# Kernel optimization log

Measured on AMD Instinct MI355X. Metric: run time of the kernel, lower is better.

The kernel has to match this reference:

```python
import jax, jax.numpy as jnp
import numpy as np

DIM = 512
HEADS = 8
DHEAD = 64
INNER = HEADS * DHEAD
CHUNK = 8
GAMMA = 1.0
EPS = 1e-8
LN_EPS = 1e-5


def setup_inputs() -> dict:
    key = jax.random.key(0)
    ks = jax.random.split(key, 10)
    B, N = 64, 256
    return {
        "q": jax.random.normal(ks[0], (B, N, DIM), jnp.float32),
        "k": jax.random.normal(ks[1], (B, N, DIM), jnp.float32),
        "v": jax.random.normal(ks[2], (B, N, DIM), jnp.float32),
        "ln_gamma": jnp.ones((DIM,), jnp.float32),
        "ln_beta": jnp.zeros((DIM,), jnp.float32),
        "W_in": jax.random.normal(ks[3], (DIM, INNER), jnp.float32) / np.sqrt(DIM),
        "W_out": jax.random.normal(ks[4], (INNER, DIM), jnp.float32) / np.sqrt(INNER),
        "b_out": jnp.zeros((DIM,), jnp.float32),
        "cov_logit": jnp.asarray(0.6, jnp.float32),
        "var_logit": jnp.asarray(0.2, jnp.float32),
        "use_advanced": 1,
    }


def _layernorm(x, g, b):
    mu = jnp.mean(x, axis=-1, keepdims=True)
    var = jnp.mean(jnp.square(x - mu), axis=-1, keepdims=True)
    return (x - mu) * jax.lax.rsqrt(var + LN_EPS) * g + b


def _transform(t, ln_gamma, ln_beta, W_in):
    # [B,N,dim] -> [h,B,N,d]
    B, N, _ = t.shape
    f = _layernorm(t, ln_gamma, ln_beta) @ W_in
    return f.reshape(B, N, HEADS, DHEAD).transpose(2, 0, 1, 3)


def _chunk_stats(E):
    # E: [M, N, d], chunks of size CHUNK over M. Returns per-chunk scalars V, C of shape [M//CHUNK].
    M, N, d = E.shape
    nc = M // CHUNK
    Ec = E.reshape(nc, CHUNK, N, d)
    # variance component: torch.var is unbiased (ddof=1) over seq dim
    sigma = jnp.sqrt(jnp.var(Ec, axis=2, ddof=1) + EPS)  # [nc, CHUNK, d]
    V = jnp.mean(jax.nn.relu(GAMMA - sigma), axis=(1, 2))  # [nc]
    # covariance component: per-sample off-diagonal energy, averaged per chunk
    centered = Ec - jnp.mean(Ec, axis=2, keepdims=True)
    cov = jnp.einsum("csni,csnj->csij", centered, centered) / (N - 1)  # [nc,CHUNK,d,d]
    total = jnp.sum(jnp.square(cov), axis=(2, 3))
    diag = jnp.sum(jnp.square(jnp.diagonal(cov, axis1=2, axis2=3)), axis=2)
    C = jnp.mean((total - diag) / d, axis=1)  # [nc]
    return V, C


def reference(q, k, v, ln_gamma, ln_beta, W_in, W_out, b_out, cov_logit, var_logit, use_advanced):
    f_q = _transform(q, ln_gamma, ln_beta, W_in)  # [h,B,N,d]
    f_k = _transform(k, ln_gamma, ln_beta, W_in)
    f_v = _transform(v, ln_gamma, ln_beta, W_in)
    h, B, N, d = f_q.shape

    # cosine similarity
    dots_qk = jnp.einsum("hbnd,hbmd->hbnm", f_q, f_k)
    qn = jnp.linalg.norm(f_q, axis=-1)  # [h,B,N]
    kn = jnp.linalg.norm(f_k, axis=-1)
    cosine_sim = dots_qk / (qn[..., :, None] * kn[..., None, :])

    if use_advanced:
        Vq, Cq = _chunk_stats(f_q.reshape(h * B, N, d))
        Vk, Ck = _chunk_stats(f_k.reshape(h * B, N, d))
        var_component = jnp.repeat(Vq * Vk, CHUNK).reshape(h, B, 1, 1)
        cov_component = jnp.repeat(Cq * Ck, CHUNK).reshape(h, B, 1, 1)
    else:
        qc = f_q - jnp.mean(f_q, axis=-1, keepdims=True)
        kc = f_k - jnp.mean(f_k, axis=-1, keepdims=True)
        cov_component = jnp.einsum("hbnd,hbmd->hbnm", qc, kc) / d
        q_var = jnp.var(f_q, axis=-1, ddof=1, keepdims=True)  # [h,B,N,1]
        k_var = jnp.var(f_k, axis=-1, ddof=1, keepdims=True)
        var_component = (q_var * jnp.swapaxes(k_var, -1, -2)) / d

    cov_w = jax.nn.sigmoid(cov_logit)
    var_w = jax.nn.sigmoid(var_logit)
    cos_w = 1.0 - cov_w - var_w
    dots = cos_w * cosine_sim + cov_w * cov_component + var_w * var_component
    out = jnp.einsum("hbnm,hbmd->hbnd", dots, f_v)
    out = out.transpose(1, 2, 0, 3).reshape(B, N, h * d)
    return out @ W_out + b_out
```

## Files before the change

### kernel.cpp

```cpp
#include <hip/hip_runtime.h>
#include <cstdint>
#include <cstddef>

#define DIM    512
#define HEADS  8
#define DHEAD  64
#define NSEQ   256
#define BATCH  64
#define NROWS  (BATCH * NSEQ)
#define HB     (HEADS * BATCH)

typedef unsigned short u16;
typedef __bf16 bf16x8 __attribute__((ext_vector_type(8)));
typedef float  f32x4  __attribute__((ext_vector_type(4)));

__device__ __forceinline__ float sigmoidf_(float x) { return 1.0f / (1.0f + expf(-x)); }

__device__ __forceinline__ u16 f2bf(float f) {
    union { float f; unsigned u; } a; a.f = f;
    return (u16)((a.u + 0x7fffu + ((a.u >> 16) & 1u)) >> 16);
}

__device__ __forceinline__ void gload16(const void* g, void* l) {
    __builtin_amdgcn_global_load_lds((const __attribute__((address_space(1))) void*)g,
                                     (__attribute__((address_space(3))) void*)l, 16, 0, 0);
}

__global__ __launch_bounds__(256)
void ln_cast_kernel(const float* __restrict__ x, const float* __restrict__ gam,
                    const float* __restrict__ bet, u16* __restrict__ out)
{
    const int wid = threadIdx.x >> 6, lane = threadIdx.x & 63;
    const int row = blockIdx.x * 4 + wid;
    const float* xr = x + (size_t)row * DIM;
    float4 a = *(const float4*)(xr + lane * 8);
    float4 b = *(const float4*)(xr + lane * 8 + 4);
    float v[8] = {a.x, a.y, a.z, a.w, b.x, b.y, b.z, b.w};
    float s = 0.f;
#pragma unroll
    for (int i = 0; i < 8; ++i) s += v[i];
#pragma unroll
    for (int o = 32; o > 0; o >>= 1) s += __shfl_xor(s, o, 64);
    const float mu = s * (1.f / DIM);
    float sq = 0.f;
#pragma unroll
    for (int i = 0; i < 8; ++i) { float d = v[i] - mu; sq += d * d; }
#pragma unroll
    for (int o = 32; o > 0; o >>= 1) sq += __shfl_xor(sq, o, 64);
    const float rstd = rsqrtf(sq * (1.f / DIM) + 1e-5f);
    float4 g0 = *(const float4*)(gam + lane * 8), g1 = *(const float4*)(gam + lane * 8 + 4);
    float4 b0 = *(const float4*)(bet + lane * 8), b1 = *(const float4*)(bet + lane * 8 + 4);
    float gv[8] = {g0.x, g0.y, g0.z, g0.w, g1.x, g1.y, g1.z, g1.w};
    float bv[8] = {b0.x, b0.y, b0.z, b0.w, b1.x, b1.y, b1.z, b1.w};
    union { u16 h[8]; uint4 u; } o16;
#pragma unroll
    for (int i = 0; i < 8; ++i) o16.h[i] = f2bf((v[i] - mu) * rstd * gv[i] + bv[i]);
    *(uint4*)(out + (size_t)row * DIM + lane * 8) = o16.u;
}

__global__ __launch_bounds__(256)
void transpose_cast_kernel(const float* __restrict__ W, u16* __restrict__ WT)
{
    __shared__ float tile[64][65];
    const int t = threadIdx.x;
    const int bx = blockIdx.x * 64, by = blockIdx.y * 64;
#pragma unroll
    for (int i = 0; i < 16; ++i) {
        int idx = i * 256 + t, r = idx >> 6, c = idx & 63;
        tile[r][c] = W[(size_t)(by + r) * DIM + bx + c];
    }
    __syncthreads();
#pragma unroll
    for (int i = 0; i < 16; ++i) {
        int idx = i * 256 + t, r = idx >> 6, c = idx & 63;
        WT[(size_t)(bx + r) * DIM + by + c] = f2bf(tile[c][r]);
    }
}

template <int MODE>
__global__ __launch_bounds__(256)
void mfma_gemm_kernel(const u16* __restrict__ A, const u16* __restrict__ BT,
                      const float* __restrict__ bias, float* __restrict__ C,
                      u16* __restrict__ FT, u16* __restrict__ Fseq)
{
    __shared__ u16 As[128 * 32];
    __shared__ u16 Bs[128 * 32];
    const int t = threadIdx.x, lane = t & 63, w = t >> 6;
    const int wr = w >> 1, wc = w & 1;
    const int r0 = blockIdx.x * 128, c0 = blockIdx.y * 128;
    const int cl = lane & 15, q = lane >> 4;

    f32x4 acc[4][4];
#pragma unroll
    for (int i = 0; i < 4; ++i)
#pragma unroll
        for (int j = 0; j < 4; ++j) acc[i][j] = (f32x4){0.f, 0.f, 0.f, 0.f};

    for (int k0 = 0; k0 < DIM; k0 += 32) {
#pragma unroll
        for (int i = 0; i < 2; ++i) {
            int idx = i * 256 + t;
            int row = idx >> 2, ch = idx & 3;
            gload16(A  + (size_t)(r0 + row) * DIM + k0 + ch * 8, As + idx * 8);
            gload16(BT + (size_t)(c0 + row) * DIM + k0 + ch * 8, Bs + idx * 8);
        }
        __syncthreads();
        bf16x8 af[4], bfr[4];
#pragma unroll
        for (int mi = 0; mi < 4; ++mi)
            af[mi] = *(const bf16x8*)(As + (wr * 64 + mi * 16 + cl) * 32 + q * 8);
#pragma unroll
        for (int ni = 0; ni < 4; ++ni)
            bfr[ni] = *(const bf16x8*)(Bs + (wc * 64 + ni * 16 + cl) * 32 + q * 8);
#pragma unroll
        for (int mi = 0; mi < 4; ++mi)
#pragma unroll
            for (int ni = 0; ni < 4; ++ni)
                acc[mi][ni] = __builtin_amdgcn_mfma_f32_16x16x32_bf16(af[mi], bfr[ni],
                                                                      acc[mi][ni], 0, 0, 0);
        __syncthreads();
    }
#pragma unroll
    for (int mi = 0; mi < 4; ++mi) {
        int row0 = r0 + wr * 64 + mi * 16 + q * 4;
#pragma unroll
        for (int ni = 0; ni < 4; ++ni) {
            int col = c0 + wc * 64 + ni * 16 + cl;
            if (MODE == 1) {
                float bv = bias[col];
#pragma unroll
                for (int r = 0; r < 4; ++r)
                    C[(size_t)(row0 + r) * DIM + col] = acc[mi][ni][r] + bv;
            } else {
                union { u16 h[4]; ushort4 u; } h4;
#pragma unroll
                for (int r = 0; r < 4; ++r) h4.h[r] = f2bf(acc[mi][ni][r]);
                int tns = row0 >> 14, b = (row0 >> 8) & 63, n = row0 & 255;
                *(ushort4*)(FT + (((size_t)(tns * 64 + b) * 512 + col) * 256 + n)) = h4.u;
                if (row0 < NROWS) {
#pragma unroll
                    for (int r = 0; r < 4; ++r)
                        Fseq[(size_t)(row0 + r) * DIM + col] = h4.h[r];
                }
            }
        }
    }
}

__global__ __launch_bounds__(256)
void stats_kernel(const u16* __restrict__ FT, float* __restrict__ norms,
                  float2* __restrict__ vc)
{
    __shared__ u16 ET[64 * 264];
    __shared__ float mu[64];
    __shared__ float red[4][64];
    __shared__ float wr3[4][3];
    const int hb = blockIdx.x, tns = blockIdx.y, h = hb >> 6, b = hb & 63;
    const int t = threadIdx.x, lane = t & 63, w = t >> 6, cl = lane & 15, q = lane >> 4;
    const size_t Fb = ((size_t)(tns * 64 + b) * 512 + h * 64) * 256;

#pragma unroll
    for (int i = 0; i < 8; ++i) {
        int idx = t + 256 * i;
        int row = idx >> 5, ch = idx & 31;
        *(bf16x8*)(ET + row * 264 + ch * 8) =
            *(const bf16x8*)(FT + Fb + (size_t)row * 256 + ch * 8);
    }
    __syncthreads();

    {
        float s = 0.f;
#pragma unroll
        for (int d = 0; d < 64; ++d) {
            float x = (float)*(const __bf16*)(ET + d * 264 + t);
            s += x * x;
        }
        norms[((size_t)tns * HB + hb) * 256 + t] = sqrtf(s);
    }
    {
        int d = t & 63, part = t >> 6;
        float s = 0.f;
#pragma unroll
        for (int i = 0; i < 8; ++i) {
            bf16x8 v8 = *(const bf16x8*)(ET + d * 264 + part * 64 + i * 8);
#pragma unroll
            for (int j = 0; j < 8; ++j) s += (float)v8[j];
        }
        red[part][d] = s;
    }
    __syncthreads();
    if (t < 64) mu[t] = (red[0][t] + red[1][t] + red[2][t] + red[3][t]) * (1.f / 256.f);
    __syncthreads();

    f32x4 g[4];
#pragma unroll
    for (int nj = 0; nj < 4; ++nj) g[nj] = (f32x4){0.f, 0.f, 0.f, 0.f};
#pragma unroll
    for (int ks = 0; ks < 8; ++ks) {
        bf16x8 af = *(const bf16x8*)(ET + (16 * w + cl) * 264 + ks * 32 + q * 8);
#pragma unroll
        for (int nj = 0; nj < 4; ++nj) {
            bf16x8 bfr = *(const bf16x8*)(ET + (16 * nj + cl) * 264 + ks * 32 + q * 8);
            g[nj] = __builtin_amdgcn_mfma_f32_16x16x32_bf16(af, bfr, g[nj], 0, 0, 0);
        }
    }
    float t2 = 0.f, d2 = 0.f, vs = 0.f;
#pragma unroll
    for (int nj = 0; nj < 4; ++nj) {
        int j = 16 * nj + cl;
        float mj = mu[j];
#pragma unroll
        for (int r = 0; r < 4; ++r) {
            int i = 16 * w + 4 * q + r;
            float gc = (g[nj][r] - 256.f * mu[i] * mj) * (1.f / 255.f);
            float g2 = gc * gc;
            t2 += g2;
            if (i == j) {
                d2 += g2;
                float sig = sqrtf(gc + 1e-8f);
                vs += fmaxf(1.f - sig, 0.f);
            }
        }
    }
#pragma unroll
    for (int o = 32; o > 0; o >>= 1) {
        t2 += __shfl_xor(t2, o, 64);
        d2 += __shfl_xor(d2, o, 64);
        vs += __shfl_xor(vs, o, 64);
    }
    if (lane == 0) { wr3[w][0] = t2; wr3[w][1] = d2; wr3[w][2] = vs; }
    __syncthreads();
    if (t == 0) {
        float T = 0.f, D = 0.f, V = 0.f;
        for (int i = 0; i < 4; ++i) { T += wr3[i][0]; D += wr3[i][1]; V += wr3[i][2]; }
        vc[(size_t)tns * HB + hb] = make_float2(V * (1.f / 64.f), (T - D) * (1.f / 64.f));
    }
}

__global__ void combine_kernel(const float2* __restrict__ vc, const float* __restrict__ cov_logit,
                               const float* __restrict__ var_logit, float* __restrict__ s_out)
{
    int hb = threadIdx.x + blockIdx.x * blockDim.x;
    if (hb >= HB) return;
    int base = hb & ~7;
    float vq = 0, cq = 0, vk = 0, ck = 0;
#pragma unroll
    for (int m = 0; m < 8; ++m) {
        float2 a = vc[base + m];      vq += a.x; cq += a.y;
        float2 b = vc[HB + base + m]; vk += b.x; ck += b.y;
    }
    float cw = sigmoidf_(*cov_logit), vw = sigmoidf_(*var_logit);
    s_out[hb] = (cw * cq * ck + vw * vq * vk) * (1.f / 64.f);
}

__global__ __launch_bounds__(256)
void attn_kernel(const u16* __restrict__ FT, const u16* __restrict__ Fseq,
                 const float* __restrict__ norms, const float* __restrict__ s_arr,
                 const float* __restrict__ cov_logit, const float* __restrict__ var_logit,
                 u16* __restrict__ G)
{
    __shared__ u16 pool[256 * 72];
    __shared__ u16 MT[64 * 72];
    __shared__ float invq[256], invk[256], sv[64];
    const int hb = blockIdx.x, h = hb >> 6, b = hb & 63;
    const int t = threadIdx.x, lane = t & 63, w = t >> 6, cl = lane & 15, q = lane >> 4;
    u16* KT = pool;
    u16* VT = pool + 64 * 136;

    invq[t] = 1.f / norms[((size_t)0 * HB + hb) * 256 + t];
    invk[t] = 1.f / norms[((size_t)1 * HB + hb) * 256 + t];
    __syncthreads();

    const size_t FTk = ((size_t)(1 * 64 + b) * 512 + h * 64) * 256;
    const size_t FTv = ((size_t)(2 * 64 + b) * 512 + h * 64) * 256;
    f32x4 acc1[4];
#pragma unroll
    for (int nj = 0; nj < 4; ++nj) acc1[nj] = (f32x4){0.f, 0.f, 0.f, 0.f};
    float sp[4] = {0.f, 0.f, 0.f, 0.f};

    for (int c = 0; c < 2; ++c) {
#pragma unroll
        for (int i = 0; i < 4; ++i) {
            int idx = t + 256 * i;
            int row = idx >> 4, ch = idx & 15;
            int n0 = c * 128 + ch * 8;
            bf16x8 kv = *(const bf16x8*)(FT + FTk + (size_t)row * 256 + n0);
            bf16x8 vv = *(const bf16x8*)(FT + FTv + (size_t)row * 256 + n0);
            bf16x8 ksc;
#pragma unroll
            for (int j = 0; j < 8; ++j) ksc[j] = (__bf16)((float)kv[j] * invk[n0 + j]);
            *(bf16x8*)(KT + row * 136 + ch * 8) = ksc;
            *(bf16x8*)(VT + row * 136 + ch * 8) = vv;
        }
        __syncthreads();
#pragma unroll
        for (int ks = 0; ks < 4; ++ks) {
            bf16x8 af = *(const bf16x8*)(KT + (16 * w + cl) * 136 + ks * 32 + q * 8);
#pragma unroll
            for (int nj = 0; nj < 4; ++nj) {
                bf16x8 bfr = *(const bf16x8*)(VT + (16 * nj + cl) * 136 + ks * 32 + q * 8);
                if (w == 0) {
                    float s = 0.f;
#pragma unroll
                    for (int j = 0; j < 8; ++j) s += (float)bfr[j];
                    sp[nj] += s;
                }
                acc1[nj] = __builtin_amdgcn_mfma_f32_16x16x32_bf16(af, bfr, acc1[nj], 0, 0, 0);
            }
        }
        __syncthreads();
    }
    if (w == 0) {
#pragma unroll
        for (int nj = 0; nj < 4; ++nj) {
            float s = sp[nj];
            s += __shfl_xor(s, 16, 64);
            s += __shfl_xor(s, 32, 64);
            if (q == 0) sv[16 * nj + cl] = s;
        }
    }
#pragma unroll
    for (int nj = 0; nj < 4; ++nj)
#pragma unroll
        for (int r = 0; r < 4; ++r)
            MT[(16 * nj + cl) * 72 + 16 * w + 4 * q + r] = f2bf(acc1[nj][r]);
    __syncthreads();

    const float cw = sigmoidf_(*cov_logit), vw = sigmoidf_(*var_logit);
    const float cosw = 1.f - cw - vw;
    const float s_hb = s_arr[hb];
    f32x4 acc2[4][4];
#pragma unroll
    for (int mi = 0; mi < 4; ++mi)
#pragma unroll
        for (int nj = 0; nj < 4; ++nj) acc2[mi][nj] = (f32x4){0.f, 0.f, 0.f, 0.f};
    const size_t Fq = (size_t)(b * 256) * DIM + h * 64;
#pragma unroll
    for (int ks2 = 0; ks2 < 2; ++ks2) {
        bf16x8 bfm[4];
#pragma unroll
        for (int nj = 0; nj < 4; ++nj)
            bfm[nj] = *(const bf16x8*)(MT + (16 * nj + cl) * 72 + ks2 * 32 + q * 8);
#pragma unroll
        for (int mi = 0; mi < 4; ++mi) {
            bf16x8 aq = *(const bf16x8*)(Fseq + Fq +
                         (size_t)(64 * w + 16 * mi + cl) * DIM + ks2 * 32 + q * 8);
#pragma unroll
            for (int nj = 0; nj < 4; ++nj)
                acc2[mi][nj] = __builtin_amdgcn_mfma_f32_16x16x32_bf16(aq, bfm[nj],
                                                                       acc2[mi][nj], 0, 0, 0);
        }
    }
    __syncthreads();
    u16* Os = pool;
#pragma unroll
    for (int mi = 0; mi < 4; ++mi) {
        int nbase = 64 * w + 16 * mi + 4 * q;
#pragma unroll
        for (int nj = 0; nj < 4; ++nj) {
            int j = 16 * nj + cl;
            float svj = sv[j];
#pragma unroll
            for (int r = 0; r < 4; ++r) {
                float o = cosw * acc2[mi][nj][r] * invq[nbase + r] + s_hb * svj;
                Os[(nbase + r) * 72 + j] = f2bf(o);
            }
        }
    }
    __syncthreads();
#pragma unroll
    for (int i = 0; i < 8; ++i) {
        int cidx = t + 256 * i;
        int row = cidx >> 3, ch = cidx & 7;
        *(uint4*)(G + (size_t)(b * 256 + row) * DIM + h * 64 + ch * 8) =
            *(const uint4*)(Os + row * 72 + ch * 8);
    }
}

extern "C" void kernel_launch(void* const* d_in, const int* in_sizes, int n_in,
                              void* d_out, int out_size, void* d_ws, size_t ws_size,
                              hipStream_t stream)
{
    const float* q         = (const float*)d_in[0];
    const float* k         = (const float*)d_in[1];
    const float* v         = (const float*)d_in[2];
    const float* ln_g      = (const float*)d_in[3];
    const float* ln_b      = (const float*)d_in[4];
    const float* W_in      = (const float*)d_in[5];
    const float* W_out     = (const float*)d_in[6];
    const float* b_out     = (const float*)d_in[7];
    const float* cov_logit = (const float*)d_in[8];
    const float* var_logit = (const float*)d_in[9];
    float* out = (float*)d_out;

    char* base = (char*)d_ws;
    u16*    Abf   = (u16*)base;
    u16*    WT    = (u16*)(base + 50331648);
    u16*    FT    = (u16*)(base + 51380224);
    u16*    Fseq  = (u16*)(base + 101711872);
    float*  norms = (float*)(base + 118489088);
    float2* vc    = (float2*)(base + 119537664);
    float*  s_arr = (float*)(base + 119545856);
    u16*    Gb    = Abf;

    transpose_cast_kernel<<<dim3(8, 8), 256, 0, stream>>>(W_in, WT);
    transpose_cast_kernel<<<dim3(8, 8), 256, 0, stream>>>(W_out, WT + 512 * 512);

    const float* in3[3] = {q, k, v};
    for (int tns = 0; tns < 3; ++tns)
        ln_cast_kernel<<<dim3(NROWS / 4), 256, 0, stream>>>(in3[tns], ln_g, ln_b,
                                                            Abf + (size_t)tns * NROWS * DIM);
    mfma_gemm_kernel<0><<<dim3(3 * NROWS / 128, 4), 256, 0, stream>>>(
        Abf, WT, nullptr, nullptr, FT, Fseq);

    stats_kernel<<<dim3(HB, 2), 256, 0, stream>>>(FT, norms, vc);
    combine_kernel<<<dim3(1), 512, 0, stream>>>(vc, cov_logit, var_logit, s_arr);
    attn_kernel<<<dim3(HB), 256, 0, stream>>>(FT, Fseq, norms, s_arr,
                                              cov_logit, var_logit, Gb);
    mfma_gemm_kernel<1><<<dim3(NROWS / 128, 4), 256, 0, stream>>>(
        Gb, WT + 512 * 512, b_out, out, nullptr, nullptr);
}
```

Baseline: 256.1 us.

## Fuse layernorm into input projection GEMM and stage epilogue stores through LDS

Removes the separate layernorm-to-bf16 kernel. The input GEMM now computes per-row mean and rstd in a prologue and normalizes fp32 activations as it loads A tiles into LDS. The GEMM epilogue stages results through a padded LDS tile so the transposed FT and sequence-major Fseq writes become coalesced 16-byte stores. The combine kernel is folded into attention and the two weight transposes are merged into one launch. The aim is to cut the bf16 activation round-trip and launch overhead, at the cost of reading each input row once per column block (4x) without async loads, plus a one-pass variance formula.

```diff
diff --git a/kernel.cpp b/kernel.cpp
--- a/kernel.cpp
+++ b/kernel.cpp
@@ -27,43 +27,14 @@
 }
 
 __global__ __launch_bounds__(256)
-void ln_cast_kernel(const float* __restrict__ x, const float* __restrict__ gam,
-                    const float* __restrict__ bet, u16* __restrict__ out)
-{
-    const int wid = threadIdx.x >> 6, lane = threadIdx.x & 63;
-    const int row = blockIdx.x * 4 + wid;
-    const float* xr = x + (size_t)row * DIM;
-    float4 a = *(const float4*)(xr + lane * 8);
-    float4 b = *(const float4*)(xr + lane * 8 + 4);
-    float v[8] = {a.x, a.y, a.z, a.w, b.x, b.y, b.z, b.w};
-    float s = 0.f;
-#pragma unroll
-    for (int i = 0; i < 8; ++i) s += v[i];
-#pragma unroll
-    for (int o = 32; o > 0; o >>= 1) s += __shfl_xor(s, o, 64);
-    const float mu = s * (1.f / DIM);
-    float sq = 0.f;
-#pragma unroll
-    for (int i = 0; i < 8; ++i) { float d = v[i] - mu; sq += d * d; }
-#pragma unroll
-    for (int o = 32; o > 0; o >>= 1) sq += __shfl_xor(sq, o, 64);
-    const float rstd = rsqrtf(sq * (1.f / DIM) + 1e-5f);
-    float4 g0 = *(const float4*)(gam + lane * 8), g1 = *(const float4*)(gam + lane * 8 + 4);
-    float4 b0 = *(const float4*)(bet + lane * 8), b1 = *(const float4*)(bet + lane * 8 + 4);
-    float gv[8] = {g0.x, g0.y, g0.z, g0.w, g1.x, g1.y, g1.z, g1.w};
-    float bv[8] = {b0.x, b0.y, b0.z, b0.w, b1.x, b1.y, b1.z, b1.w};
-    union { u16 h[8]; uint4 u; } o16;
-#pragma unroll
-    for (int i = 0; i < 8; ++i) o16.h[i] = f2bf((v[i] - mu) * rstd * gv[i] + bv[i]);
-    *(uint4*)(out + (size_t)row * DIM + lane * 8) = o16.u;
-}
-
-__global__ __launch_bounds__(256)
-void transpose_cast_kernel(const float* __restrict__ W, u16* __restrict__ WT)
+void transpose_cast_kernel(const float* __restrict__ W0, const float* __restrict__ W1,
+                           u16* __restrict__ WT)
 {
     __shared__ float tile[64][65];
     const int t = threadIdx.x;
     const int bx = blockIdx.x * 64, by = blockIdx.y * 64;
+    const float* W = blockIdx.z ? W1 : W0;
+    u16* dst = WT + (size_t)blockIdx.z * 512 * 512;
 #pragma unroll
     for (int i = 0; i < 16; ++i) {
         int idx = i * 256 + t, r = idx >> 6, c = idx & 63;
@@ -73,22 +44,54 @@
 #pragma unroll
     for (int i = 0; i < 16; ++i) {
         int idx = i * 256 + t, r = idx >> 6, c = idx & 63;
-        WT[(size_t)(bx + r) * DIM + by + c] = f2bf(tile[c][r]);
-    }
-}
-
-template <int MODE>
+        dst[(size_t)(bx + r) * DIM + by + c] = f2bf(tile[c][r]);
+    }
+}
+
 __global__ __launch_bounds__(256)
-void mfma_gemm_kernel(const u16* __restrict__ A, const u16* __restrict__ BT,
-                      const float* __restrict__ bias, float* __restrict__ C,
-                      u16* __restrict__ FT, u16* __restrict__ Fseq)
+void fused_in_gemm_kernel(const float* __restrict__ qp, const float* __restrict__ kp,
+                          const float* __restrict__ vp, const float* __restrict__ gam,
+                          const float* __restrict__ bet, const u16* __restrict__ BT,
+                          u16* __restrict__ FT, u16* __restrict__ Fseq)
 {
     __shared__ u16 As[128 * 32];
     __shared__ u16 Bs[128 * 32];
+    __shared__ u16 Ct[128 * 136];
+    __shared__ float2 lnst[128];
     const int t = threadIdx.x, lane = t & 63, w = t >> 6;
     const int wr = w >> 1, wc = w & 1;
     const int r0 = blockIdx.x * 128, c0 = blockIdx.y * 128;
-    const int cl = lane & 15, q = lane >> 4;
+    const int tns = r0 >> 14;
+    const float* X = (tns == 0) ? qp : (tns == 1) ? kp : vp;
+    const int lr0 = r0 & 16383;
+    const int cl = lane & 15, qd = lane >> 4;
+
+    {
+        const int rl = t >> 4, l16 = t & 15;
+        for (int rg = 0; rg < 8; ++rg) {
+            int row = rg * 16 + rl;
+            const float* xr = X + (size_t)(lr0 + row) * DIM;
+            float s = 0.f, sq = 0.f;
+#pragma unroll
+            for (int j2 = 0; j2 < 8; ++j2) {
+                float4 xv = *(const float4*)(xr + l16 * 4 + j2 * 64);
+                s += xv.x + xv.y + xv.z + xv.w;
+                sq += xv.x * xv.x + xv.y * xv.y + xv.z * xv.z + xv.w * xv.w;
+            }
+#pragma unroll
+            for (int o = 8; o > 0; o >>= 1) { s += __shfl_xor(s, o, 64); sq += __shfl_xor(sq, o, 64); }
+            if (l16 == 0) {
+                float mu = s * (1.f / DIM);
+                float var = sq * (1.f / DIM) - mu * mu;
+                lnst[row] = make_float2(mu, rsqrtf(var + 1e-5f));
+            }
+        }
+    }
+    __syncthreads();
+    float2 ms[4];
+#pragma unroll
+    for (int i = 0; i < 4; ++i) ms[i] = lnst[(t >> 3) + 32 * i];
+    const int c4 = (t & 7) * 4;
 
     f32x4 acc[4][4];
 #pragma unroll
@@ -97,21 +100,33 @@
         for (int j = 0; j < 4; ++j) acc[i][j] = (f32x4){0.f, 0.f, 0.f, 0.f};
 
     for (int k0 = 0; k0 < DIM; k0 += 32) {
+        float4 g4 = *(const float4*)(gam + k0 + c4);
+        float4 b4 = *(const float4*)(bet + k0 + c4);
 #pragma unroll
         for (int i = 0; i < 2; ++i) {
-            int idx = i * 256 + t;
-            int row = idx >> 2, ch = idx & 3;
-            gload16(A  + (size_t)(r0 + row) * DIM + k0 + ch * 8, As + idx * 8);
+            int idx = i * 256 + t, row = idx >> 2, ch = idx & 3;
             gload16(BT + (size_t)(c0 + row) * DIM + k0 + ch * 8, Bs + idx * 8);
         }
+#pragma unroll
+        for (int i = 0; i < 4; ++i) {
+            int row = (t >> 3) + 32 * i;
+            float4 xv = *(const float4*)(X + (size_t)(lr0 + row) * DIM + k0 + c4);
+            float2 m = ms[i];
+            union { u16 h[4]; ushort4 u; } h4;
+            h4.h[0] = f2bf((xv.x - m.x) * m.y * g4.x + b4.x);
+            h4.h[1] = f2bf((xv.y - m.x) * m.y * g4.y + b4.y);
+            h4.h[2] = f2bf((xv.z - m.x) * m.y * g4.z + b4.z);
+            h4.h[3] = f2bf((xv.w - m.x) * m.y * g4.w + b4.w);
+            *(ushort4*)(As + row * 32 + c4) = h4.u;
+        }
         __syncthreads();
         bf16x8 af[4], bfr[4];
 #pragma unroll
         for (int mi = 0; mi < 4; ++mi)
-            af[mi] = *(const bf16x8*)(As + (wr * 64 + mi * 16 + cl) * 32 + q * 8);
+            af[mi] = *(const bf16x8*)(As + (wr * 64 + mi * 16 + cl) * 32 + qd * 8);
 #pragma unroll
         for (int ni = 0; ni < 4; ++ni)
-            bfr[ni] = *(const bf16x8*)(Bs + (wc * 64 + ni * 16 + cl) * 32 + q * 8);
+            bfr[ni] = *(const bf16x8*)(Bs + (wc * 64 + ni * 16 + cl) * 32 + qd * 8);
 #pragma unroll
         for (int mi = 0; mi < 4; ++mi)
 #pragma unroll
@@ -120,30 +135,46 @@
                                                                       acc[mi][ni], 0, 0, 0);
         __syncthreads();
     }
+
+    if (tns == 0) {
+#pragma unroll
+        for (int mi = 0; mi < 4; ++mi) {
+            int lrow = wr * 64 + mi * 16 + qd * 4;
+#pragma unroll
+            for (int ni = 0; ni < 4; ++ni) {
+                int lcol = wc * 64 + ni * 16 + cl;
+#pragma unroll
+                for (int r = 0; r < 4; ++r)
+                    Ct[(lrow + r) * 136 + lcol] = f2bf(acc[mi][ni][r]);
+            }
+        }
+        __syncthreads();
+#pragma unroll
+        for (int i = 0; i < 8; ++i) {
+            int idx = t + 256 * i, row = idx >> 4, ch = idx & 15;
+            *(uint4*)(Fseq + (size_t)(lr0 + row) * DIM + c0 + ch * 8) =
+                *(const uint4*)(Ct + row * 136 + ch * 8);
+        }
+        __syncthreads();
+    }
 #pragma unroll
     for (int mi = 0; mi < 4; ++mi) {
-        int row0 = r0 + wr * 64 + mi * 16 + q * 4;
+        int lrow = wr * 64 + mi * 16 + qd * 4;
 #pragma unroll
         for (int ni = 0; ni < 4; ++ni) {
-            int col = c0 + wc * 64 + ni * 16 + cl;
-            if (MODE == 1) {
-                float bv = bias[col];
-#pragma unroll
-                for (int r = 0; r < 4; ++r)
-                    C[(size_t)(row0 + r) * DIM + col] = acc[mi][ni][r] + bv;
-            } else {
-                union { u16 h[4]; ushort4 u; } h4;
-#pragma unroll
-                for (int r = 0; r < 4; ++r) h4.h[r] = f2bf(acc[mi][ni][r]);
-                int tns = row0 >> 14, b = (row0 >> 8) & 63, n = row0 & 255;
-                *(ushort4*)(FT + (((size_t)(tns * 64 + b) * 512 + col) * 256 + n)) = h4.u;
-                if (row0 < NROWS) {
-#pragma unroll
-                    for (int r = 0; r < 4; ++r)
-                        Fseq[(size_t)(row0 + r) * DIM + col] = h4.h[r];
-                }
-            }
-        }
+            int lcol = wc * 64 + ni * 16 + cl;
+#pragma unroll
+            for (int r = 0; r < 4; ++r)
+                Ct[lcol * 136 + lrow + r] = f2bf(acc[mi][ni][r]);
+        }
+    }
+    __syncthreads();
+    const int b = (r0 >> 8) & 63, n0 = r0 & 255;
+#pragma unroll
+    for (int i = 0; i < 8; ++i) {
+        int idx = t + 256 * i, lc = idx >> 4, ch = idx & 15;
+        *(uint4*)(FT + (((size_t)(tns * 64 + b) * 512 + c0 + lc) * 256 + n0 + ch * 8)) =
+            *(const uint4*)(Ct + lc * 136 + ch * 8);
     }
 }
 
@@ -237,25 +268,9 @@
     }
 }
 
-__global__ void combine_kernel(const float2* __restrict__ vc, const float* __restrict__ cov_logit,
-                               const float* __restrict__ var_logit, float* __restrict__ s_out)
-{
-    int hb = threadIdx.x + blockIdx.x * blockDim.x;
-    if (hb >= HB) return;
-    int base = hb & ~7;
-    float vq = 0, cq = 0, vk = 0, ck = 0;
-#pragma unroll
-    for (int m = 0; m < 8; ++m) {
-        float2 a = vc[base + m];      vq += a.x; cq += a.y;
-        float2 b = vc[HB + base + m]; vk += b.x; ck += b.y;
-    }
-    float cw = sigmoidf_(*cov_logit), vw = sigmoidf_(*var_logit);
-    s_out[hb] = (cw * cq * ck + vw * vq * vk) * (1.f / 64.f);
-}
-
 __global__ __launch_bounds__(256)
 void attn_kernel(const u16* __restrict__ FT, const u16* __restrict__ Fseq,
-                 const float* __restrict__ norms, const float* __restrict__ s_arr,
+                 const float* __restrict__ norms, const float2* __restrict__ vc,
                  const float* __restrict__ cov_logit, const float* __restrict__ var_logit,
                  u16* __restrict__ G)
 {
@@ -267,6 +282,20 @@
     u16* KT = pool;
     u16* VT = pool + 64 * 136;
 
+    const float cw = sigmoidf_(*cov_logit), vw = sigmoidf_(*var_logit);
+    const float cosw = 1.f - cw - vw;
+    float s_hb;
+    {
+        int basec = hb & ~7;
+        float vq = 0, cq = 0, vk = 0, ck = 0;
+#pragma unroll
+        for (int m = 0; m < 8; ++m) {
+            float2 a = vc[basec + m];      vq += a.x; cq += a.y;
+            float2 bb = vc[HB + basec + m]; vk += bb.x; ck += bb.y;
+        }
+        s_hb = (cw * cq * ck + vw * vq * vk) * (1.f / 64.f);
+    }
+
     invq[t] = 1.f / norms[((size_t)0 * HB + hb) * 256 + t];
     invk[t] = 1.f / norms[((size_t)1 * HB + hb) * 256 + t];
     __syncthreads();
@@ -326,9 +355,7 @@
             MT[(16 * nj + cl) * 72 + 16 * w + 4 * q + r] = f2bf(acc1[nj][r]);
     __syncthreads();
 
-    const float cw = sigmoidf_(*cov_logit), vw = sigmoidf_(*var_logit);
-    const float cosw = 1.f - cw - vw;
-    const float s_hb = s_arr[hb];
+    const float s = s_hb;
     f32x4 acc2[4][4];
 #pragma unroll
     for (int mi = 0; mi < 4; ++mi)
@@ -362,7 +389,7 @@
             float svj = sv[j];
 #pragma unroll
             for (int r = 0; r < 4; ++r) {
-                float o = cosw * acc2[mi][nj][r] * invq[nbase + r] + s_hb * svj;
+                float o = cosw * acc2[mi][nj][r] * invq[nbase + r] + s * svj;
                 Os[(nbase + r) * 72 + j] = f2bf(o);
             }
         }
@@ -374,6 +401,61 @@
         int row = cidx >> 3, ch = cidx & 7;
         *(uint4*)(G + (size_t)(b * 256 + row) * DIM + h * 64 + ch * 8) =
             *(const uint4*)(Os + row * 72 + ch * 8);
+    }
+}
+
+__global__ __launch_bounds__(256)
+void out_gemm_kernel(const u16* __restrict__ A, const u16* __restrict__ BT,
+                     const float* __restrict__ bias, float* __restrict__ C)
+{
+    __shared__ u16 As[128 * 32];
+    __shared__ u16 Bs[128 * 32];
+    const int t = threadIdx.x, lane = t & 63, w = t >> 6;
+    const int wr = w >> 1, wc = w & 1;
+    const int r0 = blockIdx.x * 128, c0 = blockIdx.y * 128;
+    const int cl = lane & 15, q = lane >> 4;
+
+    f32x4 acc[4][4];
+#pragma unroll
+    for (int i = 0; i < 4; ++i)
+#pragma unroll
+        for (int j = 0; j < 4; ++j) acc[i][j] = (f32x4){0.f, 0.f, 0.f, 0.f};
+
+    for (int k0 = 0; k0 < DIM; k0 += 32) {
+#pragma unroll
+        for (int i = 0; i < 2; ++i) {
+            int idx = i * 256 + t;
+            int row = idx >> 2, ch = idx & 3;
+            gload16(A  + (size_t)(r0 + row) * DIM + k0 + ch * 8, As + idx * 8);
+            gload16(BT + (size_t)(c0 + row) * DIM + k0 + ch * 8, Bs + idx * 8);
+        }
+        __syncthreads();
+        bf16x8 af[4], bfr[4];
+#pragma unroll
+        for (int mi = 0; mi < 4; ++mi)
+            af[mi] = *(const bf16x8*)(As + (wr * 64 + mi * 16 + cl) * 32 + q * 8);
+#pragma unroll
+        for (int ni = 0; ni < 4; ++ni)
+            bfr[ni] = *(const bf16x8*)(Bs + (wc * 64 + ni * 16 + cl) * 32 + q * 8);
+#pragma unroll
+        for (int mi = 0; mi < 4; ++mi)
+#pragma unroll
+            for (int ni = 0; ni < 4; ++ni)
+                acc[mi][ni] = __builtin_amdgcn_mfma_f32_16x16x32_bf16(af[mi], bfr[ni],
+                                                                      acc[mi][ni], 0, 0, 0);
+        __syncthreads();
+    }
+#pragma unroll
+    for (int mi = 0; mi < 4; ++mi) {
+        int row0 = r0 + wr * 64 + mi * 16 + q * 4;
+#pragma unroll
+        for (int ni = 0; ni < 4; ++ni) {
+            int col = c0 + wc * 64 + ni * 16 + cl;
+            float bv = bias[col];
+#pragma unroll
+            for (int r = 0; r < 4; ++r)
+                C[(size_t)(row0 + r) * DIM + col] = acc[mi][ni][r] + bv;
+        }
     }
 }
 
@@ -394,29 +476,19 @@
     float* out = (float*)d_out;
 
     char* base = (char*)d_ws;
-    u16*    Abf   = (u16*)base;
-    u16*    WT    = (u16*)(base + 50331648);
-    u16*    FT    = (u16*)(base + 51380224);
-    u16*    Fseq  = (u16*)(base + 101711872);
-    float*  norms = (float*)(base + 118489088);
-    float2* vc    = (float2*)(base + 119537664);
-    float*  s_arr = (float*)(base + 119545856);
-    u16*    Gb    = Abf;
-
-    transpose_cast_kernel<<<dim3(8, 8), 256, 0, stream>>>(W_in, WT);
-    transpose_cast_kernel<<<dim3(8, 8), 256, 0, stream>>>(W_out, WT + 512 * 512);
-
-    const float* in3[3] = {q, k, v};
-    for (int tns = 0; tns < 3; ++tns)
-        ln_cast_kernel<<<dim3(NROWS / 4), 256, 0, stream>>>(in3[tns], ln_g, ln_b,
-                                                            Abf + (size_t)tns * NROWS * DIM);
-    mfma_gemm_kernel<0><<<dim3(3 * NROWS / 128, 4), 256, 0, stream>>>(
-        Abf, WT, nullptr, nullptr, FT, Fseq);
-
+    u16*    Gb    = (u16*)base;
+    u16*    WT    = (u16*)(base + 16777216);
+    u16*    FT    = (u16*)(base + 17825792);
+    u16*    Fseq  = (u16*)(base + 68157440);
+    float*  norms = (float*)(base + 84934656);
+    float2* vc    = (float2*)(base + 85983232);
+
+    transpose_cast_kernel<<<dim3(8, 8, 2), 256, 0, stream>>>(W_in, W_out, WT);
+    fused_in_gemm_kernel<<<dim3(3 * NROWS / 128, 4), 256, 0, stream>>>(
+        q, k, v, ln_g, ln_b, WT, FT, Fseq);
     stats_kernel<<<dim3(HB, 2), 256, 0, stream>>>(FT, norms, vc);
-    combine_kernel<<<dim3(1), 512, 0, stream>>>(vc, cov_logit, var_logit, s_arr);
-    attn_kernel<<<dim3(HB), 256, 0, stream>>>(FT, Fseq, norms, s_arr,
+    attn_kernel<<<dim3(HB), 256, 0, stream>>>(FT, Fseq, norms, vc,
                                               cov_logit, var_logit, Gb);
-    mfma_gemm_kernel<1><<<dim3(NROWS / 128, 4), 256, 0, stream>>>(
-        Gb, WT + 512 * 512, b_out, out, nullptr, nullptr);
-}
+    out_gemm_kernel<<<dim3(NROWS / 128, 4), 256, 0, stream>>>(
+        Gb, WT + 512 * 512, b_out, out);
+}
```

Result: slower. 293.0 us (+14.4%).
